# Optimization experiments

Measured on AMD Instinct MI355X. Metric: run time of the kernel, lower is better.

## Reference

```python
import jax, jax.numpy as jnp
import numpy as np

N_NODES = 50000
N_EDGES = 600000
D_IN = 128
D_HID = 128


def setup_inputs() -> dict:
    key = jax.random.key(0)
    ks = jax.random.split(key, 12)
    edge_index = jax.random.randint(ks[0], (2, N_EDGES), 0, N_NODES)
    x = jax.random.normal(ks[1], (N_NODES, D_IN), dtype=jnp.float32)
    shuffled_x = jax.random.normal(ks[2], (N_NODES, D_IN), dtype=jnp.float32)
    # DIMPLayer params: linear transform applied after neighbor aggregation
    sc = 1.0 / np.sqrt(D_IN)
    W0 = jax.random.uniform(ks[3], (D_IN, D_HID), jnp.float32, -sc, sc)
    b0 = jnp.zeros((D_HID,), jnp.float32)
    W1 = jax.random.uniform(ks[4], (D_HID, D_HID), jnp.float32, -sc, sc)
    b1 = jnp.zeros((D_HID,), jnp.float32)
    W2 = jax.random.uniform(ks[5], (D_HID, D_HID), jnp.float32, -sc, sc)
    b2 = jnp.zeros((D_HID,), jnp.float32)
    # Bilinear discriminator weight
    Wd = jax.random.uniform(ks[6], (D_HID, D_HID), jnp.float32, -sc, sc)
    return {"edge_index": edge_index, "x": x, "shuffled_x": shuffled_x,
            "W0": W0, "b0": b0, "W1": W1, "b1": b1, "W2": W2, "b2": b2,
            "Wd": Wd}


def reference(edge_index, x, shuffled_x, W0, b0, W1, b1, W2, b2, Wd):
    src, dst = edge_index[0], edge_index[1]
    n = x.shape[0]

    def dimp_layer(h, W, b):
        # gather source-node features along edges, scatter-add into destinations
        agg = jax.ops.segment_sum(h[src], dst, num_segments=n)  # [N, d]
        return jax.nn.relu(agg @ W + b)

    params = [(W0, b0), (W1, b1), (W2, b2)]

    def encode(feat):
        h = feat
        for W, b in params:
            h = dimp_layer(h, W, b)
        return h

    h = encode(x)                    # [N, D_HID]
    s = jnp.mean(h, axis=0)          # [D_HID] graph summary
    shuffled_h = encode(shuffled_x)  # [N, D_HID]

    # Bilinear discriminator: logit_i = h_i^T Wd s
    ws = Wd @ s                      # [D_HID]
    d_h = h @ ws                     # [N]
    d_shuffled_h = shuffled_h @ ws   # [N]
    return jnp.concatenate((d_h, d_shuffled_h), axis=0)  # [2N]
```

## Files before the change

kernel.cpp:

```cpp
#include <hip/hip_runtime.h>

#define D 128

typedef short bf16x8 __attribute__((ext_vector_type(8)));
typedef float f32x4 __attribute__((ext_vector_type(4)));

static __device__ __forceinline__ unsigned short f2bf(float f) {
    unsigned int u = __float_as_uint(f);
    u = u + 0x7FFFu + ((u >> 16) & 1u);
    return (unsigned short)(u >> 16);
}
static __device__ __forceinline__ float bf2f(unsigned short h) {
    return __uint_as_float(((unsigned int)h) << 16);
}


__global__ __launch_bounds__(256) void count_kernel(const int* __restrict__ dst,
        int* __restrict__ counts, int E) {
    int e = blockIdx.x * 256 + threadIdx.x;
    if (e < E) atomicAdd(&counts[dst[e]], 1);
}

__global__ __launch_bounds__(256) void scan_reduce(const int* __restrict__ counts,
        int* __restrict__ bsum, int n) {
    int b = blockIdx.x, t = threadIdx.x;
    int base = b * 1024 + t * 4;
    int s = 0;
    #pragma unroll
    for (int i = 0; i < 4; ++i) {
        int idx = base + i;
        if (idx < n) s += counts[idx];
    }
    __shared__ int sd[256];
    sd[t] = s;
    __syncthreads();
    #pragma unroll
    for (int off = 128; off > 0; off >>= 1) {
        if (t < off) sd[t] += sd[t + off];
        __syncthreads();
    }
    if (t == 0) bsum[b] = sd[0];
}

__global__ __launch_bounds__(64) void scan_tops(const int* __restrict__ bsum,
        int* __restrict__ bofs, int* __restrict__ row_ptr_end, int B) {
    int t = threadIdx.x;
    int v = (t < B) ? bsum[t] : 0;
    int inc = v;
    #pragma unroll
    for (int off = 1; off < 64; off <<= 1) {
        int u = __shfl_up(inc, off);
        if (t >= off) inc += u;
    }
    if (t < B) bofs[t] = inc - v;
    if (t == 63) *row_ptr_end = inc;
}

__global__ __launch_bounds__(256) void scan_final(const int* __restrict__ counts,
        const int* __restrict__ bofs, int* __restrict__ row_ptr,
        int* __restrict__ cursor, int n) {
    int b = blockIdx.x, t = threadIdx.x;
    int base = b * 1024 + t * 4;
    int v[4];
    int s = 0;
    #pragma unroll
    for (int i = 0; i < 4; ++i) {
        int idx = base + i;
        v[i] = (idx < n) ? counts[idx] : 0;
        s += v[i];
    }
    __shared__ int sd[256];
    sd[t] = s;
    __syncthreads();
    #pragma unroll
    for (int off = 1; off < 256; off <<= 1) {
        int u = (t >= off) ? sd[t - off] : 0;
        __syncthreads();
        sd[t] += u;
        __syncthreads();
    }
    int excl = bofs[b] + sd[t] - s;
    #pragma unroll
    for (int i = 0; i < 4; ++i) {
        int idx = base + i;
        if (idx < n) {
            row_ptr[idx] = excl;
            cursor[idx] = excl;
            excl += v[i];
        }
    }
}

__global__ __launch_bounds__(256) void fill_kernel(const int* __restrict__ src,
        const int* __restrict__ dst, int* __restrict__ cursor,
        int* __restrict__ src_sorted, int E) {
    int e = blockIdx.x * 256 + threadIdx.x;
    if (e < E) {
        int p = atomicAdd(&cursor[dst[e]], 1);
        src_sorted[p] = src[e];
    }
}


__global__ __launch_bounds__(256) void cvt_kernel(const float* __restrict__ in,
        unsigned short* __restrict__ out, int n4) {
    int i = blockIdx.x * 256 + threadIdx.x;
    if (i < n4) {
        float4 v = ((const float4*)in)[i];
        ushort4 o;
        o.x = f2bf(v.x); o.y = f2bf(v.y); o.z = f2bf(v.z); o.w = f2bf(v.w);
        ((ushort4*)out)[i] = o;
    }
}


__global__ __launch_bounds__(256) void pack_w(const float* __restrict__ W,
        unsigned short* __restrict__ Wp) {
    int t = blockIdx.x * 256 + threadIdx.x;
    if (t >= 2048) return;
    int lane = t & 63;
    int ct = (t >> 6) & 7;
    int s = t >> 9;
    int n = ct * 16 + (lane & 15);
    int k0 = s * 32 + (lane >> 4) * 8;
    unsigned short hi[8], lo[8];
    #pragma unroll
    for (int j = 0; j < 8; ++j) {
        float f = W[(size_t)(k0 + j) * 128 + n];
        unsigned short h = f2bf(f);
        hi[j] = h;
        lo[j] = f2bf(f - bf2f(h));
    }
    size_t bh = ((size_t)((s * 8 + ct) * 2 + 0) * 64 + lane) * 8;
    size_t bl = ((size_t)((s * 8 + ct) * 2 + 1) * 64 + lane) * 8;
    #pragma unroll
    for (int j = 0; j < 8; ++j) { Wp[bh + j] = hi[j]; Wp[bl + j] = lo[j]; }
}


__global__ __launch_bounds__(256) void agg_kernel(const unsigned short* __restrict__ h,
        const int* __restrict__ row_ptr, const int* __restrict__ src_sorted,
        float* __restrict__ out, int N, int NT) {
    int node = blockIdx.x * 16 + (threadIdx.x >> 4);
    int lane = threadIdx.x & 15;
    if (node >= NT) return;
    int base = (node < N) ? 0 : N;
    int rp = node - base;
    int beg = row_ptr[rp], end = row_ptr[rp + 1];
    const uint4* h4 = (const uint4*)h;

    float acc[8];
    #pragma unroll
    for (int i = 0; i < 8; ++i) acc[i] = 0.f;

    auto addrow = [&](uint4 v) {
        acc[0] += __uint_as_float(v.x << 16);
        acc[1] += __uint_as_float(v.x & 0xFFFF0000u);
        acc[2] += __uint_as_float(v.y << 16);
        acc[3] += __uint_as_float(v.y & 0xFFFF0000u);
        acc[4] += __uint_as_float(v.z << 16);
        acc[5] += __uint_as_float(v.z & 0xFFFF0000u);
        acc[6] += __uint_as_float(v.w << 16);
        acc[7] += __uint_as_float(v.w & 0xFFFF0000u);
    };

    int j = beg;
    for (; j + 3 < end; j += 4) {
        int s0 = src_sorted[j] + base;
        int s1 = src_sorted[j + 1] + base;
        int s2 = src_sorted[j + 2] + base;
        int s3 = src_sorted[j + 3] + base;
        uint4 v0 = h4[(size_t)s0 * 16 + lane];
        uint4 v1 = h4[(size_t)s1 * 16 + lane];
        uint4 v2 = h4[(size_t)s2 * 16 + lane];
        uint4 v3 = h4[(size_t)s3 * 16 + lane];
        addrow(v0); addrow(v1); addrow(v2); addrow(v3);
    }
    for (; j < end; ++j) {
        int s0 = src_sorted[j] + base;
        addrow(h4[(size_t)s0 * 16 + lane]);
    }

    float4 f0 = make_float4(acc[0], acc[1], acc[2], acc[3]);
    float4 f1 = make_float4(acc[4], acc[5], acc[6], acc[7]);
    float4* o4 = (float4*)out;
    o4[(size_t)node * 32 + lane * 2]     = f0;
    o4[(size_t)node * 32 + lane * 2 + 1] = f1;
}


__global__ __launch_bounds__(256) void gemm_mfma(const float* __restrict__ A,
        const unsigned short* __restrict__ Wp, const float* __restrict__ bias,
        unsigned short* __restrict__ O, int M,
        float* __restrict__ mean_out, int Nmean, float inv_n) {
    __shared__ float red[4][128];
    int tid = threadIdx.x;
    int w = tid >> 6, l = tid & 63;
    int m0 = blockIdx.x * 64 + w * 16;
    int fr = l & 15;
    int kg = l >> 4;

    f32x4 acc[8];
    #pragma unroll
    for (int ct = 0; ct < 8; ++ct) acc[ct] = (f32x4){0.f, 0.f, 0.f, 0.f};

    int arow = m0 + fr; if (arow >= M) arow = M - 1;
    const float* abase = &A[(size_t)arow * 128 + kg * 8];
    const uint4* wp4 = (const uint4*)Wp;

    for (int s = 0; s < 4; ++s) {
        float4 a0 = *(const float4*)(abase + s * 32);
        float4 a1 = *(const float4*)(abase + s * 32 + 4);
        float av[8] = {a0.x, a0.y, a0.z, a0.w, a1.x, a1.y, a1.z, a1.w};
        bf16x8 a_hi, a_lo;
        #pragma unroll
        for (int j = 0; j < 8; ++j) {
            unsigned short h = f2bf(av[j]);
            a_hi[j] = (short)h;
            a_lo[j] = (short)f2bf(av[j] - bf2f(h));
        }
        #pragma unroll
        for (int ct = 0; ct < 8; ++ct) {
            uint4 bhu = wp4[(size_t)((s * 8 + ct) * 2 + 0) * 64 + l];
            uint4 blu = wp4[(size_t)((s * 8 + ct) * 2 + 1) * 64 + l];
            bf16x8 b_hi, b_lo;
            *(uint4*)&b_hi = bhu;
            *(uint4*)&b_lo = blu;
            acc[ct] = __builtin_amdgcn_mfma_f32_16x16x32_bf16(a_hi, b_hi, acc[ct], 0, 0, 0);
            acc[ct] = __builtin_amdgcn_mfma_f32_16x16x32_bf16(a_lo, b_hi, acc[ct], 0, 0, 0);
            acc[ct] = __builtin_amdgcn_mfma_f32_16x16x32_bf16(a_hi, b_lo, acc[ct], 0, 0, 0);
        }
    }

    float colsum[8];
    #pragma unroll
    for (int ct = 0; ct < 8; ++ct) {
        int col = ct * 16 + fr;
        float b = bias[col];
        float cs = 0.f;
        #pragma unroll
        for (int r = 0; r < 4; ++r) {
            int m = m0 + kg * 4 + r;
            float v = fmaxf(acc[ct][r] + b, 0.f);
            if (m < M) O[(size_t)m * 128 + col] = f2bf(v);
            if (m < Nmean) cs += v;
        }
        colsum[ct] = cs;
    }

    if (mean_out) {
        #pragma unroll
        for (int ct = 0; ct < 8; ++ct) {
            float v = colsum[ct];
            v += __shfl_xor(v, 16);
            v += __shfl_xor(v, 32);
            if (l < 16) red[w][ct * 16 + l] = v;
        }
        __syncthreads();
        if (tid < 128) {
            float s = red[0][tid] + red[1][tid] + red[2][tid] + red[3][tid];
            if (s != 0.f) atomicAdd(&mean_out[tid], s * inv_n);
        }
    }
}


__global__ __launch_bounds__(128) void wd_kernel(const float* __restrict__ Wd,
        const float* __restrict__ s, float* __restrict__ wsv) {
    __shared__ float sl[128];
    int i = threadIdx.x;
    sl[i] = s[i];
    __syncthreads();
    float acc = 0.f;
    for (int j = 0; j < 128; ++j) acc += Wd[(size_t)i * 128 + j] * sl[j];
    wsv[i] = acc;
}


__global__ __launch_bounds__(256) void disc_kernel(const unsigned short* __restrict__ h,
        const float* __restrict__ wsv, float* __restrict__ out, int n) {
    int wave = threadIdx.x >> 6, lane = threadIdx.x & 63;
    int node = blockIdx.x * 4 + wave;
    if (node >= n) return;
    unsigned int hv = ((const unsigned int*)h)[(size_t)node * 64 + lane];
    float2 wv = *(const float2*)&wsv[lane * 2];
    float lo = __uint_as_float(hv << 16);
    float hi = __uint_as_float(hv & 0xFFFF0000u);
    float acc = lo * wv.x + hi * wv.y;
    #pragma unroll
    for (int off = 32; off > 0; off >>= 1) acc += __shfl_down(acc, off);
    if (lane == 0) out[node] = acc;
}


extern "C" void kernel_launch(void* const* d_in, const int* in_sizes, int n_in,
                              void* d_out, int out_size, void* d_ws, size_t ws_size,
                              hipStream_t stream) {
    const int* edge_index = (const int*)d_in[0];
    const float* x  = (const float*)d_in[1];
    const float* sx = (const float*)d_in[2];
    const float* W0 = (const float*)d_in[3];
    const float* b0 = (const float*)d_in[4];
    const float* W1 = (const float*)d_in[5];
    const float* b1 = (const float*)d_in[6];
    const float* W2 = (const float*)d_in[7];
    const float* b2 = (const float*)d_in[8];
    const float* Wd = (const float*)d_in[9];
    float* out = (float*)d_out;

    const int E = in_sizes[0] / 2;
    const int N = in_sizes[1] / D;
    const int* src = edge_index;
    const int* dst = edge_index + E;
    const float inv_n = 1.0f / (float)N;

    char* wsp = (char*)d_ws;
    size_t off = 0;
    auto alloc = [&](size_t bytes) -> void* {
        void* p = wsp + off;
        off += (bytes + 511) & ~(size_t)511;
        return p;
    };
    int* counts     = (int*)alloc((size_t)N * 4);
    int* row_ptr    = (int*)alloc((size_t)(N + 1) * 4);
    int* cursor     = (int*)alloc((size_t)N * 4);
    int* src_sorted = (int*)alloc((size_t)E * 4);
    int* bsum       = (int*)alloc(64 * 4);
    int* bofs       = (int*)alloc(64 * 4);
    float* svec     = (float*)alloc(D * 4);
    float* wsv      = (float*)alloc(D * 4);
    unsigned short* wp0 = (unsigned short*)alloc((size_t)D * D * 2 * 2);
    unsigned short* wp1 = (unsigned short*)alloc((size_t)D * D * 2 * 2);
    unsigned short* wp2 = (unsigned short*)alloc((size_t)D * D * 2 * 2);

    size_t fixed = off;
    size_t need_batched = fixed + ((size_t)2 * N * D * 4 + 512) + ((size_t)2 * N * D * 2 + 512);
    bool batched = ws_size >= need_batched;
    int NB = batched ? 2 * N : N;

    float* aggbuf        = (float*)alloc((size_t)NB * D * 4);
    unsigned short* hbuf = (unsigned short*)alloc((size_t)NB * D * 2);

    hipMemsetAsync(counts, 0, (size_t)N * 4, stream);
    hipMemsetAsync(svec, 0, D * 4, stream);

    pack_w<<<8, 256, 0, stream>>>(W0, wp0);
    pack_w<<<8, 256, 0, stream>>>(W1, wp1);
    pack_w<<<8, 256, 0, stream>>>(W2, wp2);

    int eblocks = (E + 255) / 256;
    int sblocks = (N + 1023) / 1024;
    count_kernel<<<eblocks, 256, 0, stream>>>(dst, counts, E);
    scan_reduce<<<sblocks, 256, 0, stream>>>(counts, bsum, N);
    scan_tops<<<1, 64, 0, stream>>>(bsum, bofs, row_ptr + N, sblocks);
    scan_final<<<sblocks, 256, 0, stream>>>(counts, bofs, row_ptr, cursor, N);
    fill_kernel<<<eblocks, 256, 0, stream>>>(src, dst, cursor, src_sorted, E);

    int n4 = N * D / 4;
    int cblocks = (n4 + 255) / 256;
    int ablocks = (NB + 15) / 16;
    int gblocks = (NB + 63) / 64;

    if (batched) {
        cvt_kernel<<<cblocks, 256, 0, stream>>>(x, hbuf, n4);
        cvt_kernel<<<cblocks, 256, 0, stream>>>(sx, hbuf + (size_t)N * D, n4);
        agg_kernel<<<ablocks, 256, 0, stream>>>(hbuf, row_ptr, src_sorted, aggbuf, N, NB);
        gemm_mfma<<<gblocks, 256, 0, stream>>>(aggbuf, wp0, b0, hbuf, NB, nullptr, 0, 0.f);
        agg_kernel<<<ablocks, 256, 0, stream>>>(hbuf, row_ptr, src_sorted, aggbuf, N, NB);
        gemm_mfma<<<gblocks, 256, 0, stream>>>(aggbuf, wp1, b1, hbuf, NB, nullptr, 0, 0.f);
        agg_kernel<<<ablocks, 256, 0, stream>>>(hbuf, row_ptr, src_sorted, aggbuf, N, NB);
        gemm_mfma<<<gblocks, 256, 0, stream>>>(aggbuf, wp2, b2, hbuf, NB, svec, N, inv_n);
        wd_kernel<<<1, 128, 0, stream>>>(Wd, svec, wsv);
        disc_kernel<<<(NB + 3) / 4, 256, 0, stream>>>(hbuf, wsv, out, NB);
    } else {
        auto encode = [&](const float* input, float* mean_out) {
            cvt_kernel<<<cblocks, 256, 0, stream>>>(input, hbuf, n4);
            agg_kernel<<<ablocks, 256, 0, stream>>>(hbuf, row_ptr, src_sorted, aggbuf, N, NB);
            gemm_mfma<<<gblocks, 256, 0, stream>>>(aggbuf, wp0, b0, hbuf, NB, nullptr, 0, 0.f);
            agg_kernel<<<ablocks, 256, 0, stream>>>(hbuf, row_ptr, src_sorted, aggbuf, N, NB);
            gemm_mfma<<<gblocks, 256, 0, stream>>>(aggbuf, wp1, b1, hbuf, NB, nullptr, 0, 0.f);
            agg_kernel<<<ablocks, 256, 0, stream>>>(hbuf, row_ptr, src_sorted, aggbuf, N, NB);
            gemm_mfma<<<gblocks, 256, 0, stream>>>(aggbuf, wp2, b2, hbuf, NB, mean_out, mean_out ? N : 0, inv_n);
        };
        encode(x, svec);
        wd_kernel<<<1, 128, 0, stream>>>(Wd, svec, wsv);
        disc_kernel<<<(NB + 3) / 4, 256, 0, stream>>>(hbuf, wsv, out, NB);
        encode(sx, nullptr);
        disc_kernel<<<(NB + 3) / 4, 256, 0, stream>>>(hbuf, wsv, out + N, NB);
    }
}
```

Baseline: 365.6 us.

## Fuse neighbor aggregation into MFMA GEMM with ping-pong bf16 buffers

Merges the gather/segment-sum kernel into the GEMM kernel, so each lane gathers its node's neighbor rows straight into registers laid out as MFMA A-fragments. This removes the fp32 aggregation buffer round trip through global memory and one launch per layer. Input and output must now be separate, so two bf16 buffers alternate between layers. The trade-off is the gather pattern: each lane handles one node, with 4 lanes sharing a row's 16-byte chunks strided by 4, which can coalesce worse than the old 16-lanes-per-row layout. It also uses more registers for the 32 accumulators.

```diff
diff --git a/kernel.cpp b/kernel.cpp
--- a/kernel.cpp
+++ b/kernel.cpp
@@ -138,60 +138,10 @@
 }
 
 
-__global__ __launch_bounds__(256) void agg_kernel(const unsigned short* __restrict__ h,
+__global__ __launch_bounds__(256) void agg_gemm(const unsigned short* __restrict__ Hin,
         const int* __restrict__ row_ptr, const int* __restrict__ src_sorted,
-        float* __restrict__ out, int N, int NT) {
-    int node = blockIdx.x * 16 + (threadIdx.x >> 4);
-    int lane = threadIdx.x & 15;
-    if (node >= NT) return;
-    int base = (node < N) ? 0 : N;
-    int rp = node - base;
-    int beg = row_ptr[rp], end = row_ptr[rp + 1];
-    const uint4* h4 = (const uint4*)h;
-
-    float acc[8];
-    #pragma unroll
-    for (int i = 0; i < 8; ++i) acc[i] = 0.f;
-
-    auto addrow = [&](uint4 v) {
-        acc[0] += __uint_as_float(v.x << 16);
-        acc[1] += __uint_as_float(v.x & 0xFFFF0000u);
-        acc[2] += __uint_as_float(v.y << 16);
-        acc[3] += __uint_as_float(v.y & 0xFFFF0000u);
-        acc[4] += __uint_as_float(v.z << 16);
-        acc[5] += __uint_as_float(v.z & 0xFFFF0000u);
-        acc[6] += __uint_as_float(v.w << 16);
-        acc[7] += __uint_as_float(v.w & 0xFFFF0000u);
-    };
-
-    int j = beg;
-    for (; j + 3 < end; j += 4) {
-        int s0 = src_sorted[j] + base;
-        int s1 = src_sorted[j + 1] + base;
-        int s2 = src_sorted[j + 2] + base;
-        int s3 = src_sorted[j + 3] + base;
-        uint4 v0 = h4[(size_t)s0 * 16 + lane];
-        uint4 v1 = h4[(size_t)s1 * 16 + lane];
-        uint4 v2 = h4[(size_t)s2 * 16 + lane];
-        uint4 v3 = h4[(size_t)s3 * 16 + lane];
-        addrow(v0); addrow(v1); addrow(v2); addrow(v3);
-    }
-    for (; j < end; ++j) {
-        int s0 = src_sorted[j] + base;
-        addrow(h4[(size_t)s0 * 16 + lane]);
-    }
-
-    float4 f0 = make_float4(acc[0], acc[1], acc[2], acc[3]);
-    float4 f1 = make_float4(acc[4], acc[5], acc[6], acc[7]);
-    float4* o4 = (float4*)out;
-    o4[(size_t)node * 32 + lane * 2]     = f0;
-    o4[(size_t)node * 32 + lane * 2 + 1] = f1;
-}
-
-
-__global__ __launch_bounds__(256) void gemm_mfma(const float* __restrict__ A,
         const unsigned short* __restrict__ Wp, const float* __restrict__ bias,
-        unsigned short* __restrict__ O, int M,
+        unsigned short* __restrict__ Hout, int N, int NT,
         float* __restrict__ mean_out, int Nmean, float inv_n) {
     __shared__ float red[4][128];
     int tid = threadIdx.x;
@@ -200,24 +150,61 @@
     int fr = l & 15;
     int kg = l >> 4;
 
+    int node = m0 + fr; if (node >= NT) node = NT - 1;
+    int base = (node < N) ? 0 : N;
+    int rp = node - base;
+    int beg = row_ptr[rp], end = row_ptr[rp + 1];
+
+    float acc_g[4][8];
+    #pragma unroll
+    for (int s = 0; s < 4; ++s)
+        #pragma unroll
+        for (int j = 0; j < 8; ++j) acc_g[s][j] = 0.f;
+
+    const uint4* h4 = (const uint4*)Hin;
+
+    auto addv = [&](float* a, uint4 v) {
+        a[0] += __uint_as_float(v.x << 16);
+        a[1] += __uint_as_float(v.x & 0xFFFF0000u);
+        a[2] += __uint_as_float(v.y << 16);
+        a[3] += __uint_as_float(v.y & 0xFFFF0000u);
+        a[4] += __uint_as_float(v.z << 16);
+        a[5] += __uint_as_float(v.z & 0xFFFF0000u);
+        a[6] += __uint_as_float(v.w << 16);
+        a[7] += __uint_as_float(v.w & 0xFFFF0000u);
+    };
+
+    int j = beg;
+    for (; j + 1 < end; j += 2) {
+        int s0 = src_sorted[j] + base;
+        int s1 = src_sorted[j + 1] + base;
+        const uint4* r0 = h4 + (size_t)s0 * 16 + kg;
+        const uint4* r1 = h4 + (size_t)s1 * 16 + kg;
+        uint4 a0 = r0[0], a1 = r0[4], a2 = r0[8], a3 = r0[12];
+        uint4 c0 = r1[0], c1 = r1[4], c2 = r1[8], c3 = r1[12];
+        addv(acc_g[0], a0); addv(acc_g[1], a1); addv(acc_g[2], a2); addv(acc_g[3], a3);
+        addv(acc_g[0], c0); addv(acc_g[1], c1); addv(acc_g[2], c2); addv(acc_g[3], c3);
+    }
+    if (j < end) {
+        int s0 = src_sorted[j] + base;
+        const uint4* r0 = h4 + (size_t)s0 * 16 + kg;
+        uint4 a0 = r0[0], a1 = r0[4], a2 = r0[8], a3 = r0[12];
+        addv(acc_g[0], a0); addv(acc_g[1], a1); addv(acc_g[2], a2); addv(acc_g[3], a3);
+    }
+
     f32x4 acc[8];
     #pragma unroll
     for (int ct = 0; ct < 8; ++ct) acc[ct] = (f32x4){0.f, 0.f, 0.f, 0.f};
 
-    int arow = m0 + fr; if (arow >= M) arow = M - 1;
-    const float* abase = &A[(size_t)arow * 128 + kg * 8];
     const uint4* wp4 = (const uint4*)Wp;
-
     for (int s = 0; s < 4; ++s) {
-        float4 a0 = *(const float4*)(abase + s * 32);
-        float4 a1 = *(const float4*)(abase + s * 32 + 4);
-        float av[8] = {a0.x, a0.y, a0.z, a0.w, a1.x, a1.y, a1.z, a1.w};
         bf16x8 a_hi, a_lo;
         #pragma unroll
-        for (int j = 0; j < 8; ++j) {
-            unsigned short h = f2bf(av[j]);
-            a_hi[j] = (short)h;
-            a_lo[j] = (short)f2bf(av[j] - bf2f(h));
+        for (int jj = 0; jj < 8; ++jj) {
+            float f = acc_g[s][jj];
+            unsigned short h = f2bf(f);
+            a_hi[jj] = (short)h;
+            a_lo[jj] = (short)f2bf(f - bf2f(h));
         }
         #pragma unroll
         for (int ct = 0; ct < 8; ++ct) {
@@ -242,7 +229,7 @@
         for (int r = 0; r < 4; ++r) {
             int m = m0 + kg * 4 + r;
             float v = fmaxf(acc[ct][r] + b, 0.f);
-            if (m < M) O[(size_t)m * 128 + col] = f2bf(v);
+            if (m < NT) Hout[(size_t)m * 128 + col] = f2bf(v);
             if (m < Nmean) cs += v;
         }
         colsum[ct] = cs;
@@ -334,12 +321,12 @@
     unsigned short* wp2 = (unsigned short*)alloc((size_t)D * D * 2 * 2);
 
     size_t fixed = off;
-    size_t need_batched = fixed + ((size_t)2 * N * D * 4 + 512) + ((size_t)2 * N * D * 2 + 512);
+    size_t need_batched = fixed + 2 * ((size_t)2 * N * D * 2 + 512);
     bool batched = ws_size >= need_batched;
     int NB = batched ? 2 * N : N;
 
-    float* aggbuf        = (float*)alloc((size_t)NB * D * 4);
-    unsigned short* hbuf = (unsigned short*)alloc((size_t)NB * D * 2);
+    unsigned short* hbufA = (unsigned short*)alloc((size_t)NB * D * 2);
+    unsigned short* hbufB = (unsigned short*)alloc((size_t)NB * D * 2);
 
     hipMemsetAsync(counts, 0, (size_t)N * 4, stream);
     hipMemsetAsync(svec, 0, D * 4, stream);
@@ -358,34 +345,33 @@
 
     int n4 = N * D / 4;
     int cblocks = (n4 + 255) / 256;
-    int ablocks = (NB + 15) / 16;
     int gblocks = (NB + 63) / 64;
 
     if (batched) {
-        cvt_kernel<<<cblocks, 256, 0, stream>>>(x, hbuf, n4);
-        cvt_kernel<<<cblocks, 256, 0, stream>>>(sx, hbuf + (size_t)N * D, n4);
-        agg_kernel<<<ablocks, 256, 0, stream>>>(hbuf, row_ptr, src_sorted, aggbuf, N, NB);
-        gemm_mfma<<<gblocks, 256, 0, stream>>>(aggbuf, wp0, b0, hbuf, NB, nullptr, 0, 0.f);
-        agg_kernel<<<ablocks, 256, 0, stream>>>(hbuf, row_ptr, src_sorted, aggbuf, N, NB);
-        gemm_mfma<<<gblocks, 256, 0, stream>>>(aggbuf, wp1, b1, hbuf, NB, nullptr, 0, 0.f);
-        agg_kernel<<<ablocks, 256, 0, stream>>>(hbuf, row_ptr, src_sorted, aggbuf, N, NB);
-        gemm_mfma<<<gblocks, 256, 0, stream>>>(aggbuf, wp2, b2, hbuf, NB, svec, N, inv_n);
+        cvt_kernel<<<cblocks, 256, 0, stream>>>(x, hbufA, n4);
+        cvt_kernel<<<cblocks, 256, 0, stream>>>(sx, hbufA + (size_t)N * D, n4);
+        agg_gemm<<<gblocks, 256, 0, stream>>>(hbufA, row_ptr, src_sorted, wp0, b0,
+                                              hbufB, N, NB, nullptr, 0, 0.f);
+        agg_gemm<<<gblocks, 256, 0, stream>>>(hbufB, row_ptr, src_sorted, wp1, b1,
+                                              hbufA, N, NB, nullptr, 0, 0.f);
+        agg_gemm<<<gblocks, 256, 0, stream>>>(hbufA, row_ptr, src_sorted, wp2, b2,
+                                              hbufB, N, NB, svec, N, inv_n);
         wd_kernel<<<1, 128, 0, stream>>>(Wd, svec, wsv);
-        disc_kernel<<<(NB + 3) / 4, 256, 0, stream>>>(hbuf, wsv, out, NB);
+        disc_kernel<<<(NB + 3) / 4, 256, 0, stream>>>(hbufB, wsv, out, NB);
     } else {
         auto encode = [&](const float* input, float* mean_out) {
-            cvt_kernel<<<cblocks, 256, 0, stream>>>(input, hbuf, n4);
-            agg_kernel<<<ablocks, 256, 0, stream>>>(hbuf, row_ptr, src_sorted, aggbuf, N, NB);
-            gemm_mfma<<<gblocks, 256, 0, stream>>>(aggbuf, wp0, b0, hbuf, NB, nullptr, 0, 0.f);
-            agg_kernel<<<ablocks, 256, 0, stream>>>(hbuf, row_ptr, src_sorted, aggbuf, N, NB);
-            gemm_mfma<<<gblocks, 256, 0, stream>>>(aggbuf, wp1, b1, hbuf, NB, nullptr, 0, 0.f);
-            agg_kernel<<<ablocks, 256, 0, stream>>>(hbuf, row_ptr, src_sorted, aggbuf, N, NB);
-            gemm_mfma<<<gblocks, 256, 0, stream>>>(aggbuf, wp2, b2, hbuf, NB, mean_out, mean_out ? N : 0, inv_n);
+            cvt_kernel<<<cblocks, 256, 0, stream>>>(input, hbufA, n4);
+            agg_gemm<<<gblocks, 256, 0, stream>>>(hbufA, row_ptr, src_sorted, wp0, b0,
+                                                  hbufB, N, NB, nullptr, 0, 0.f);
+            agg_gemm<<<gblocks, 256, 0, stream>>>(hbufB, row_ptr, src_sorted, wp1, b1,
+                                                  hbufA, N, NB, nullptr, 0, 0.f);
+            agg_gemm<<<gblocks, 256, 0, stream>>>(hbufA, row_ptr, src_sorted, wp2, b2,
+                                                  hbufB, N, NB, mean_out, mean_out ? N : 0, inv_n);
         };
         encode(x, svec);
         wd_kernel<<<1, 128, 0, stream>>>(Wd, svec, wsv);
-        disc_kernel<<<(NB + 3) / 4, 256, 0, stream>>>(hbuf, wsv, out, NB);
+        disc_kernel<<<(NB + 3) / 4, 256, 0, stream>>>(hbufB, wsv, out, NB);
         encode(sx, nullptr);
-        disc_kernel<<<(NB + 3) / 4, 256, 0, stream>>>(hbuf, wsv, out + N, NB);
-    }
-}
+        disc_kernel<<<(NB + 3) / 4, 256, 0, stream>>>(hbufB, wsv, out + N, NB);
+    }
+}
```

Result: slower. 384.3 us (+5.1%).
